# Performance work log

Measured on AMD Instinct MI355X. Metric: run time of the kernel, lower is better.

Reference implementation:

```python
import jax, jax.numpy as jnp
import numpy as np

# Lorentz hyperboloid with curvature -1 (k = 1): <x,x>_L = -1/k, x0 = time coord.
K_CURV = 1.0
EPS = 1e-8
B, N, D, H = 4, 1024, 1024, 16
HD = D // H  # dim_per_head = 64 (space dims per head)


def _time(space):
    # time coord so the point lies on the hyperboloid
    return jnp.sqrt(jnp.sum(space * space, axis=-1, keepdims=True) + 1.0 / K_CURV)


def _lift(space):
    return jnp.concatenate([_time(space), space], axis=-1)


def _linner(u, v):
    # Minkowski inner product <u,v>_L = -u0 v0 + u_s . v_s
    return jnp.sum(u[..., 1:] * v[..., 1:], axis=-1) - u[..., 0] * v[..., 0]


def _lorentz_layernorm(x, gamma, beta):
    s = x[..., 1:]
    mu = jnp.mean(s, axis=-1, keepdims=True)
    var = jnp.mean((s - mu) ** 2, axis=-1, keepdims=True)
    s = (s - mu) / jnp.sqrt(var + 1e-5) * gamma + beta
    return _lift(s)


def _lorentz_linear(x, W, b):
    # linear on the full Lorentz point -> space part of output, time recomputed
    return _lift(x @ W + b)


def _lresnet(x, y, w):
    # Lorentzian residual: (x + w*y) renormalized back onto the hyperboloid
    z = x + w * y
    denom = jnp.sqrt(jnp.clip(-_linner(z, z), EPS))[..., None]
    return z / (jnp.sqrt(K_CURV) * denom)


def _attention(x, Wq, bq, Wk, bk, Wv, bv, Wo, bo):
    def heads(W, b):
        s = (x @ W + b).reshape(B, N, H, HD).transpose(0, 2, 1, 3)  # [B,H,N,HD]
        return _lift(s)  # per-head Lorentz points [B,H,N,HD+1]

    q, k, v = heads(Wq, bq), heads(Wk, bk), heads(Wv, bv)
    sgn = jnp.concatenate([-jnp.ones((1,), x.dtype), jnp.ones((HD,), x.dtype)])
    # pairwise Minkowski inner products; score = -d_L^2 = 2/k + 2<q,k>_L, scaled
    scores = jnp.einsum('bhqd,bhkd->bhqk', q * sgn, k)
    scores = (2.0 / K_CURV + 2.0 * scores) / np.sqrt(HD).astype(np.float32)
    attn = jax.nn.softmax(scores, axis=-1)
    # Lorentz midpoint aggregation of values
    mid = jnp.einsum('bhqk,bhkd->bhqd', attn, v)
    denom = jnp.sqrt(jnp.clip(-_linner(mid, mid), EPS))[..., None]
    mid = mid / (jnp.sqrt(K_CURV) * denom)  # [B,H,N,HD+1]
    cat = mid.transpose(0, 2, 1, 3).reshape(B, N, H * (HD + 1))  # trans_heads_concat
    return _lift(cat @ Wo + bo)


def reference(x, g1, b1, Wq, bq, Wk, bk, Wv, bv, Wo, bo, g2, b2, Wfc, bfc, Wpj, bpj, w1, w2):
    lx = _lorentz_layernorm(x, g1, b1)
    ax = _attention(lx, Wq, bq, Wk, bk, Wv, bv, Wo, bo)
    x = _lresnet(x, ax, w1)
    h = _lorentz_layernorm(x, g2, b2)
    h = _lorentz_linear(h, Wfc, bfc)                      # [B,N,4D]
    h = _lift(jax.nn.gelu(h[..., 1:], approximate=False))  # LorentzActivation(GELU)
    h = _lorentz_linear(h, Wpj, bpj)                      # [B,N,D]
    return _lresnet(x, h, w2)


def setup_inputs() -> dict:
    key = jax.random.key(0)
    ks = jax.random.split(key, 8)
    sc = 0.02
    f32 = jnp.float32
    xs = jax.random.normal(ks[0], (B, N, D - 1), f32)
    return dict(
        x=_lift(xs),
        g1=jnp.ones((D - 1,), f32), b1=jnp.zeros((D - 1,), f32),
        Wq=sc * jax.random.normal(ks[1], (D, H * HD), f32), bq=jnp.zeros((H * HD,), f32),
        Wk=sc * jax.random.normal(ks[2], (D, H * HD), f32), bk=jnp.zeros((H * HD,), f32),
        Wv=sc * jax.random.normal(ks[3], (D, H * HD), f32), bv=jnp.zeros((H * HD,), f32),
        Wo=sc * jax.random.normal(ks[4], (H * (HD + 1), D - 1), f32), bo=jnp.zeros((D - 1,), f32),
        g2=jnp.ones((D - 1,), f32), b2=jnp.zeros((D - 1,), f32),
        Wfc=sc * jax.random.normal(ks[5], (D, 4 * D - 1), f32), bfc=jnp.zeros((4 * D - 1,), f32),
        Wpj=sc * jax.random.normal(ks[6], (4 * D, D - 1), f32), bpj=jnp.zeros((D - 1,), f32),
        w1=jnp.ones((), f32), w2=jnp.ones((), f32),
    )
```

## Files before the change

kernel.cpp:

```cpp
#include <hip/hip_runtime.h>
#include <math.h>

#define BB 4
#define NN 1024
#define DD 1024
#define HH 16
#define ROWS (BB*NN)

typedef __attribute__((ext_vector_type(8))) short bf16x8;
typedef __attribute__((ext_vector_type(4))) float f32x4;
typedef unsigned short u16;

__device__ __forceinline__ u16 f2bf(float f) {
    union { float f; unsigned u; } v; v.f = f;
    unsigned r = v.u + 0x7fff + ((v.u >> 16) & 1);
    return (u16)(r >> 16);
}
__device__ __forceinline__ float bf2f(u16 u) {
    union { unsigned u; float f; } v; v.u = ((unsigned)u) << 16; return v.f;
}

__device__ __forceinline__ void async16(const void* g, void* l) {
    __builtin_amdgcn_global_load_lds(
        (__attribute__((address_space(1))) void*)(uintptr_t)g,
        (__attribute__((address_space(3))) void*)(uintptr_t)l,
        16, 0, 0);
}

__device__ __forceinline__ float block_reduce_sum(float v, float* sm) {
    #pragma unroll
    for (int o = 32; o > 0; o >>= 1) v += __shfl_down(v, o);
    int lane = threadIdx.x & 63, wid = threadIdx.x >> 6;
    if (lane == 0) sm[wid] = v;
    __syncthreads();
    if (wid == 0) {
        v = (lane < (int)(blockDim.x >> 6)) ? sm[lane] : 0.f;
        #pragma unroll
        for (int o = 2; o > 0; o >>= 1) v += __shfl_down(v, o);
        if (lane == 0) sm[0] = v;
    }
    __syncthreads();
    float r = sm[0];
    __syncthreads();
    return r;
}

__global__ __launch_bounds__(256) void k_pre(
        const float* __restrict__ Wq_, const float* __restrict__ Wk_,
        const float* __restrict__ Wv_, const float* __restrict__ Wo_,
        const float* __restrict__ Wfc_, const float* __restrict__ Wpj_,
        u16* __restrict__ WqkvT, u16* __restrict__ WoT,
        u16* __restrict__ WfcT, u16* __restrict__ WpjT,
        const float* __restrict__ x, const float* __restrict__ g1,
        const float* __restrict__ be1, u16* __restrict__ lnout) {
    __shared__ float t[32][33];
    int bid = blockIdx.x;
    if (bid < 12352) {
        const float* W; u16* out; int K, N, Kpad, Npad, gx;
        if (bid < 1024)      { W = Wq_;  out = WqkvT;            K = 1024; N = 1024; Kpad = 1024; Npad = 1024; gx = 32; }
        else if (bid < 2048) { W = Wk_;  out = WqkvT + 1048576;  K = 1024; N = 1024; Kpad = 1024; Npad = 1024; gx = 32; bid -= 1024; }
        else if (bid < 3072) { W = Wv_;  out = WqkvT + 2097152;  K = 1024; N = 1024; Kpad = 1024; Npad = 1024; gx = 32; bid -= 2048; }
        else if (bid < 4160) { W = Wo_;  out = WoT;              K = 1040; N = 1023; Kpad = 1088; Npad = 1024; gx = 34; bid -= 3072; }
        else if (bid < 8256) { W = Wfc_; out = WfcT;             K = 1024; N = 4095; Kpad = 1024; Npad = 4096; gx = 32; bid -= 4160; }
        else                 { W = Wpj_; out = WpjT;             K = 4096; N = 1023; Kpad = 4096; Npad = 1024; gx = 128; bid -= 8256; }
        int k0 = (bid % gx) * 32, n0 = (bid / gx) * 32;
        int tx = threadIdx.x & 31, ty = threadIdx.x >> 5;
        #pragma unroll
        for (int i = 0; i < 32; i += 8) {
            int k = k0 + ty + i, n = n0 + tx;
            t[ty + i][tx] = (k < K && n < N) ? W[(size_t)k * N + n] : 0.f;
        }
        __syncthreads();
        #pragma unroll
        for (int i = 0; i < 32; i += 8) {
            int n = n0 + ty + i, k = k0 + tx;
            if (n < Npad && k < Kpad) out[(size_t)n * Kpad + k] = f2bf(t[tx][ty + i]);
        }
    } else {
        float* sm = &t[0][0];
        int row = bid - 12352;
        const float* xr = x + (size_t)row * DD;
        u16* orow = lnout + (size_t)row * DD;
        float s = 0.f, ss = 0.f;
        for (int j = threadIdx.x; j < DD - 1; j += blockDim.x) {
            float v = xr[1 + j]; s += v; ss += v * v;
        }
        s = block_reduce_sum(s, sm);
        ss = block_reduce_sum(ss, sm);
        float mu = s / (float)(DD - 1);
        float var = ss / (float)(DD - 1) - mu * mu;
        float rstd = rsqrtf(var + 1e-5f);
        float s2 = 0.f;
        for (int j = threadIdx.x; j < DD - 1; j += blockDim.x) {
            float v = (xr[1 + j] - mu) * rstd * g1[j] + be1[j];
            orow[1 + j] = f2bf(v); s2 += v * v;
        }
        s2 = block_reduce_sum(s2, sm);
        if (threadIdx.x == 0) orow[0] = f2bf(sqrtf(s2 + 1.f));
    }
}


__device__ __forceinline__ void cstore(float* p, float v) { *p = v; }
__device__ __forceinline__ void cstore(u16* p, float v) { *p = f2bf(v); }

template <typename OT>
__global__ __launch_bounds__(256) void k_gemm_mfma(
        const u16* __restrict__ A, const u16* __restrict__ BT,
        const float* __restrict__ bias, int nbias,
        OT* __restrict__ C0, OT* __restrict__ C1,
        int ldc, int ldab, int ksplit, int K) {
    __shared__ __align__(16) u16 As[128 * 64];
    __shared__ __align__(16) u16 Bs[128 * 64];
    int z = blockIdx.z;
    int kbeg = z ? ksplit : 0;
    int kend = z ? K : ksplit;
    OT* C = z ? C1 : C0;
    const float* bs = z ? nullptr : bias;

    int tiles_n = gridDim.x;
    int lin = blockIdx.y * tiles_n + blockIdx.x;
    int width = 8 * tiles_n;
    int group = lin / width;
    int rem = lin - group * width;
    int mm = group * 8 + (rem & 7);
    int nn = rem >> 3;
    int n0 = nn * 128, m0 = mm * 128;

    int tid = threadIdx.x;
    int wave = tid >> 6, lane = tid & 63;
    int quad = lane >> 4, m16 = lane & 15;
    int wm = (wave & 1) * 64, wn = (wave >> 1) * 64;

    f32x4 acc[4][4];
    #pragma unroll
    for (int t = 0; t < 4; ++t)
        #pragma unroll
        for (int u = 0; u < 4; ++u) acc[t][u] = (f32x4){0.f, 0.f, 0.f, 0.f};

    int r8 = lane >> 3;
    int cc = (lane & 7) ^ r8;
    int srow = wave * 32 + r8;
    const u16* ag = A  + (size_t)(m0 + srow) * ldab + cc * 8;
    const u16* bg = BT + (size_t)(n0 + srow) * ldab + cc * 8;
    u16* asl = &As[(wave * 32) * 64];
    u16* bsl = &Bs[(wave * 32) * 64];

    for (int k0 = kbeg; k0 < kend; k0 += 64) {
        __syncthreads();
        #pragma unroll
        for (int j = 0; j < 4; ++j) {
            async16(ag + (size_t)(j * 8) * ldab + k0, asl + (j * 8) * 64);
            async16(bg + (size_t)(j * 8) * ldab + k0, bsl + (j * 8) * 64);
        }
        __syncthreads();
        #pragma unroll
        for (int kk = 0; kk < 2; ++kk) {
            bf16x8 af[4], bfr[4];
            #pragma unroll
            for (int t = 0; t < 4; ++t) {
                int slot = (kk * 4 + quad) ^ (m16 & 7);
                af[t] = *(const bf16x8*)&As[(wm + t * 16 + m16) * 64 + slot * 8];
            }
            #pragma unroll
            for (int u = 0; u < 4; ++u) {
                int slot = (kk * 4 + quad) ^ (m16 & 7);
                bfr[u] = *(const bf16x8*)&Bs[(wn + u * 16 + m16) * 64 + slot * 8];
            }
            #pragma unroll
            for (int t = 0; t < 4; ++t)
                #pragma unroll
                for (int u = 0; u < 4; ++u)
                    acc[t][u] = __builtin_amdgcn_mfma_f32_16x16x32_bf16(af[t], bfr[u], acc[t][u], 0, 0, 0);
        }
    }
    #pragma unroll
    for (int u = 0; u < 4; ++u) {
        int col = n0 + wn + u * 16 + m16;
        float bv = (bs != nullptr && col < nbias) ? bs[col] : 0.f;
        #pragma unroll
        for (int t = 0; t < 4; ++t) {
            #pragma unroll
            for (int r = 0; r < 4; ++r) {
                int row = m0 + wm + t * 16 + quad * 4 + r;
                cstore(C + (size_t)row * ldc + col, acc[t][u][r] + bv);
            }
        }
    }
}

__global__ __launch_bounds__(256) void k_build_heads(
        const u16* __restrict__ qkv,
        const float* __restrict__ bq, const float* __restrict__ bk,
        const float* __restrict__ bv,
        u16* __restrict__ Qp, u16* __restrict__ Kp, u16* __restrict__ V2) {
    int wid = threadIdx.x >> 6, lane = threadIdx.x & 63;
    int idx = blockIdx.x * 4 + wid;
    int h = idx & 15, bn = idx >> 4;
    int b = bn >> 10, n = bn & 1023;
    int sec = blockIdx.y;
    const float* bias = (sec == 0) ? bq : (sec == 1) ? bk : bv;
    float v = bf2f(qkv[(size_t)bn * 3072 + sec * 1024 + h * 64 + lane]) + bias[h * 64 + lane];
    float ss = v * v;
    #pragma unroll
    for (int o = 32; o > 0; o >>= 1) ss += __shfl_xor(ss, o);
    float tcomp = sqrtf(ss + 1.f);
    size_t bhn = (size_t)(b * 16 + h) * 1024 + n;
    if (sec == 0) {
        u16* drow = Qp + bhn * 96;
        drow[1 + lane] = f2bf(v);
        if (lane == 0) drow[0] = f2bf(-tcomp);
        if (lane < 31) drow[65 + lane] = 0;
    } else if (sec == 1) {
        u16* drow = Kp + bhn * 104;
        drow[1 + lane] = f2bf(v);
        if (lane == 0) drow[0] = f2bf(tcomp);
        if (lane < 39) drow[65 + lane] = 0;
    } else {
        u16* base = V2 + ((size_t)(b * 16 + h) * 16 + (n >> 6)) * 6144 + (n & 63);
        base[(1 + lane) * 72] = f2bf(v);
        if (lane == 0) base[0] = f2bf(tcomp);
        if (lane >= 49) base[(16 + lane) * 72] = 0;
    }
}

#define AKS 104
#define AVS 72
#define APS 88
#define KTILE_U16 (64 * AKS)
#define VTILE_U16 6144
#define EXPC 0.36067376f
__global__ __launch_bounds__(256) void k_attn_mfma(
        const u16* __restrict__ Qp, const u16* __restrict__ Kp,
        const u16* __restrict__ V2, u16* __restrict__ cat) {
    __shared__ __align__(16) u16 Klds[2][KTILE_U16];
    __shared__ __align__(16) u16 Vlds[2][VTILE_U16];
    __shared__ __align__(16) u16 Plds[4][16 * APS];
    int tid = threadIdx.x;
    int wave = tid >> 6, lane = tid & 63;
    int quad = lane >> 4, m = lane & 15;
    int bh = blockIdx.y, qt = blockIdx.x;

    const u16* kg = Kp + (size_t)bh * 16 * KTILE_U16;
    const u16* vg = V2 + (size_t)bh * 16 * VTILE_U16;

    bf16x8 aq[2][3];
    #pragma unroll
    for (int g = 0; g < 2; ++g) {
        const u16* qptr = Qp + ((size_t)bh * 1024 + qt * 128 + g * 64 + wave * 16 + m) * 96;
        aq[g][0] = *(const bf16x8*)(qptr + quad * 8);
        aq[g][1] = *(const bf16x8*)(qptr + 32 + quad * 8);
        aq[g][2] = *(const bf16x8*)(qptr + 64 + quad * 8);
    }

    f32x4 O[2][5];
    #pragma unroll
    for (int g = 0; g < 2; ++g)
        #pragma unroll
        for (int i = 0; i < 5; ++i) O[g][i] = (f32x4){0.f, 0.f, 0.f, 0.f};

    auto stage = [&](int kt, int s) {
        const u16* kt_p = kg + kt * KTILE_U16 + lane * 8;
        const u16* vt_p = vg + kt * VTILE_U16 + lane * 8;
        for (int i = wave; i < 25; i += 4) {
            if (i < 13) async16(kt_p + i * 512, &Klds[s][i * 512]);
            else        async16(vt_p + (i - 13) * 512, &Vlds[s][(i - 13) * 512]);
        }
    };

    stage(0, 0);
    for (int kt = 0; kt < 16; ++kt) {
        int cur = kt & 1;
        __syncthreads();
        if (kt < 15) stage(kt + 1, cur ^ 1);
        u16* pw = &Plds[wave][0];
        #pragma unroll
        for (int g = 0; g < 2; ++g) {
            #pragma unroll
            for (int nt = 0; nt < 4; ++nt) {
                f32x4 acc = (f32x4){0.f, 0.f, 0.f, 0.f};
                const u16* kr = &Klds[cur][(nt * 16 + m) * AKS + quad * 8];
                acc = __builtin_amdgcn_mfma_f32_16x16x32_bf16(aq[g][0], *(const bf16x8*)(kr),      acc, 0, 0, 0);
                acc = __builtin_amdgcn_mfma_f32_16x16x32_bf16(aq[g][1], *(const bf16x8*)(kr + 32), acc, 0, 0, 0);
                acc = __builtin_amdgcn_mfma_f32_16x16x32_bf16(aq[g][2], *(const bf16x8*)(kr + 64), acc, 0, 0, 0);
                #pragma unroll
                for (int r = 0; r < 4; ++r) {
                    float p = __builtin_amdgcn_exp2f(fmaf(acc[r], EXPC, EXPC));
                    union { float f; unsigned u; } pv; pv.f = p;
                    pw[(quad * 4 + r) * APS + nt * 16 + m] = (u16)((pv.u + 0x8000u) >> 16);
                }
            }
            #pragma unroll
            for (int kc = 0; kc < 2; ++kc) {
                bf16x8 ap = *(const bf16x8*)&Plds[wave][m * APS + kc * 32 + quad * 8];
                #pragma unroll
                for (int vt = 0; vt < 5; ++vt) {
                    bf16x8 bv = *(const bf16x8*)&Vlds[cur][(vt * 16 + m) * AVS + kc * 32 + quad * 8];
                    O[g][vt] = __builtin_amdgcn_mfma_f32_16x16x32_bf16(ap, bv, O[g][vt], 0, 0, 0);
                }
            }
        }
    }
    int b = bh >> 4, h = bh & 15;
    #pragma unroll
    for (int g = 0; g < 2; ++g) {
        #pragma unroll
        for (int r = 0; r < 4; ++r) {
            float part = 0.f;
            #pragma unroll
            for (int vt = 0; vt < 5; ++vt) {
                int c = vt * 16 + m;
                float o = O[g][vt][r];
                part += (c == 0) ? o * o : -o * o;
            }
            part += __shfl_xor(part, 1);
            part += __shfl_xor(part, 2);
            part += __shfl_xor(part, 4);
            part += __shfl_xor(part, 8);
            float rden = rsqrtf(fmaxf(part, 1e-8f));
            int n = qt * 128 + g * 64 + wave * 16 + quad * 4 + r;
            u16* crow = cat + (size_t)(b * 1024 + n) * 1088 + h * 65;
            #pragma unroll
            for (int vt = 0; vt < 5; ++vt) {
                int c = vt * 16 + m;
                if (c < 65) crow[c] = f2bf(O[g][vt][r] * rden);
            }
        }
    }
    if (h == 15) {
        for (int i = tid; i < 128 * 48; i += 256) {
            int rr = i / 48, c = i - rr * 48;
            int n = qt * 128 + rr;
            cat[(size_t)(b * 1024 + n) * 1088 + 1040 + c] = 0;
        }
    }
}

__global__ __launch_bounds__(256) void k_lresnet_ln(
        const float* __restrict__ x, const float* __restrict__ y0,
        const float* __restrict__ y1, const float* __restrict__ wscale,
        const float* __restrict__ g2, const float* __restrict__ be2,
        float* __restrict__ x1, u16* __restrict__ lnout) {
    __shared__ float sm[8];
    int row = blockIdx.x;
    const float* xr = x + (size_t)row * DD;
    const float* ya = y0 + (size_t)row * 1024;
    const float* yb = y1 + (size_t)row * 1024;
    float w = *wscale;
    float zreg[4];
    float sy = 0.f, sz = 0.f, szs = 0.f;
    int cnt = 0;
    for (int j = threadIdx.x; j < DD - 1; j += blockDim.x) {
        float yv = ya[j] + yb[j];
        float zv = xr[1 + j] + w * yv;
        sy += yv * yv; sz += zv * zv; szs += zv;
        zreg[cnt++] = zv;
    }
    sy = block_reduce_sum(sy, sm);
    sz = block_reduce_sum(sz, sm);
    szs = block_reduce_sum(szs, sm);
    float y0t = sqrtf(sy + 1.f);
    float z0 = xr[0] + w * y0t;
    float q = z0 * z0 - sz;
    float rden = rsqrtf(fmaxf(q, 1e-8f));
    float mu = rden * szs / (float)(DD - 1);
    float ex2 = rden * rden * sz / (float)(DD - 1);
    float var = ex2 - mu * mu;
    float rstd = rsqrtf(var + 1e-5f);
    float s2 = 0.f;
    cnt = 0;
    float* x1r = x1 + (size_t)row * DD;
    u16* lr = lnout + (size_t)row * DD;
    for (int j = threadIdx.x; j < DD - 1; j += blockDim.x) {
        float xv = zreg[cnt++] * rden;
        x1r[1 + j] = xv;
        float v = (xv - mu) * rstd * g2[j] + be2[j];
        lr[1 + j] = f2bf(v); s2 += v * v;
    }
    s2 = block_reduce_sum(s2, sm);
    if (threadIdx.x == 0) {
        x1r[0] = z0 * rden;
        lr[0] = f2bf(sqrtf(s2 + 1.f));
    }
}

__global__ __launch_bounds__(256) void k_lresnet(
        const float* __restrict__ x, const float* __restrict__ y0,
        const float* __restrict__ y1, const float* __restrict__ wscale,
        float* __restrict__ out) {
    __shared__ float sm[8];
    int row = blockIdx.x;
    const float* xr = x + (size_t)row * DD;
    const float* ya = y0 + (size_t)row * 1024;
    const float* yb = y1 + (size_t)row * 1024;
    float w = *wscale;
    float zreg[4];
    float sy = 0.f, sz = 0.f;
    int cnt = 0;
    for (int j = threadIdx.x; j < DD - 1; j += blockDim.x) {
        float yv = ya[j] + yb[j];
        float zv = xr[1 + j] + w * yv;
        sy += yv * yv; sz += zv * zv;
        zreg[cnt++] = zv;
    }
    sy = block_reduce_sum(sy, sm);
    sz = block_reduce_sum(sz, sm);
    float y0t = sqrtf(sy + 1.f);
    float z0 = xr[0] + w * y0t;
    float q = z0 * z0 - sz;
    float rden = rsqrtf(fmaxf(q, 1e-8f));
    cnt = 0;
    for (int j = threadIdx.x; j < DD - 1; j += blockDim.x)
        out[(size_t)row * DD + 1 + j] = zreg[cnt++] * rden;
    if (threadIdx.x == 0) out[(size_t)row * DD] = z0 * rden;
}

__global__ __launch_bounds__(256) void k_gelu_lift(
        const u16* __restrict__ hfc, u16* __restrict__ hg) {
    __shared__ float sm[8];
    int row = blockIdx.x;
    const u16* hr = hfc + (size_t)row * 4096;
    u16* gr = hg + (size_t)row * 4096;
    float s2 = 0.f;
    for (int j = threadIdx.x; j < 4095; j += blockDim.x) {
        float v = bf2f(hr[j]);
        float gl = 0.5f * v * (1.f + erff(v * 0.70710678f));
        gr[1 + j] = f2bf(gl); s2 += gl * gl;
    }
    s2 = block_reduce_sum(s2, sm);
    if (threadIdx.x == 0) gr[0] = f2bf(sqrtf(s2 + 1.f));
}

extern "C" void kernel_launch(void* const* d_in, const int* in_sizes, int n_in,
                              void* d_out, int out_size, void* d_ws, size_t ws_size,
                              hipStream_t stream) {
    const float* x   = (const float*)d_in[0];
    const float* g1  = (const float*)d_in[1];
    const float* b1  = (const float*)d_in[2];
    const float* Wq  = (const float*)d_in[3];
    const float* bq  = (const float*)d_in[4];
    const float* Wk  = (const float*)d_in[5];
    const float* bk  = (const float*)d_in[6];
    const float* Wv  = (const float*)d_in[7];
    const float* bv  = (const float*)d_in[8];
    const float* Wo  = (const float*)d_in[9];
    const float* bo  = (const float*)d_in[10];
    const float* g2  = (const float*)d_in[11];
    const float* b2  = (const float*)d_in[12];
    const float* Wfc = (const float*)d_in[13];
    const float* bfc = (const float*)d_in[14];
    const float* Wpj = (const float*)d_in[15];
    const float* bpj = (const float*)d_in[16];
    const float* w1  = (const float*)d_in[17];
    const float* w2  = (const float*)d_in[18];
    float* out = (float*)d_out;

    char* W = (char*)d_ws;
    u16* lx_bf  = (u16*)(W + 0);
    u16* WqkvT  = (u16*)(W + 8388608);
    u16* WoT    = (u16*)(W + 14680064);
    u16* WfcT   = (u16*)(W + 16908288);
    u16* WpjT   = (u16*)(W + 25296896);
    u16* qkv_bf = (u16*)(W + 33685504);
    u16* Qp     = (u16*)(W + 58851328);
    u16* Kp     = (u16*)(W + 71434240);
    u16* V2     = (u16*)(W + 85065728);
    u16* cat_bf = (u16*)(W + 97648640);
    float* ax0  = (float*)(W + 33685504);
    float* ax1  = (float*)(W + 50462720);
    float* x1   = (float*)(W + 67239936);
    u16* hfc_bf = (u16*)(W + 84017152);
    u16* hg_bf  = (u16*)(W + 33685504);
    float* h2a  = (float*)(W + 84017152);
    float* h2b  = (float*)(W + 100794368);

    dim3 blk(256);

    k_pre<<<16448, blk, 0, stream>>>(Wq, Wk, Wv, Wo, Wfc, Wpj,
                                     WqkvT, WoT, WfcT, WpjT,
                                     x, g1, b1, lx_bf);

    k_gemm_mfma<u16><<<dim3(24, 32, 1), blk, 0, stream>>>(
        lx_bf, WqkvT, nullptr, 0, qkv_bf, qkv_bf, 3072, 1024, 1024, 1024);
    k_build_heads<<<dim3(ROWS * HH / 4, 3), blk, 0, stream>>>(
        qkv_bf, bq, bk, bv, Qp, Kp, V2);

    k_attn_mfma<<<dim3(8, 64), blk, 0, stream>>>(Qp, Kp, V2, cat_bf);

    k_gemm_mfma<float><<<dim3(8, 32, 2), blk, 0, stream>>>(
        cat_bf, WoT, bo, 1023, ax0, ax1, 1024, 1088, 576, 1088);

    k_lresnet_ln<<<ROWS, blk, 0, stream>>>(x, ax0, ax1, w1, g2, b2, x1, lx_bf);

    k_gemm_mfma<u16><<<dim3(32, 32, 1), blk, 0, stream>>>(
        lx_bf, WfcT, bfc, 4095, hfc_bf, hfc_bf, 4096, 1024, 1024, 1024);

    k_gelu_lift<<<ROWS, blk, 0, stream>>>(hfc_bf, hg_bf);

    k_gemm_mfma<float><<<dim3(8, 32, 2), blk, 0, stream>>>(
        hg_bf, WpjT, bpj, 1023, h2a, h2b, 1024, 4096, 2048, 4096);

    k_lresnet<<<ROWS, blk, 0, stream>>>(x1, h2a, h2b, w2, out);
}
```

Measured before the change: 446.6 us.

## Double-buffer LDS tiles in MFMA GEMM and drop grouped tile ordering

Splits the GEMM's shared-memory A/B tiles into two stages. The global-to-LDS async load for the next K-tile is issued right after a single barrier, so it overlaps the MFMA work on the current tile; this removes one barrier per iteration and hides load latency. It also replaces the grouped (8-row super-tile) block-to-tile mapping with plain blockIdx mapping, which may reduce L2 reuse across neighbouring blocks. The doubled LDS footprint (64 KB per block) can lower occupancy.

```diff
diff --git a/kernel.cpp b/kernel.cpp
--- a/kernel.cpp
+++ b/kernel.cpp
@@ -100,7 +100,6 @@
     }
 }
 
-
 __device__ __forceinline__ void cstore(float* p, float v) { *p = v; }
 __device__ __forceinline__ void cstore(u16* p, float v) { *p = f2bf(v); }
 
@@ -110,26 +109,18 @@
         const float* __restrict__ bias, int nbias,
         OT* __restrict__ C0, OT* __restrict__ C1,
         int ldc, int ldab, int ksplit, int K) {
-    __shared__ __align__(16) u16 As[128 * 64];
-    __shared__ __align__(16) u16 Bs[128 * 64];
+    __shared__ __align__(16) u16 As[2][128 * 64];
+    __shared__ __align__(16) u16 Bs[2][128 * 64];
     int z = blockIdx.z;
     int kbeg = z ? ksplit : 0;
     int kend = z ? K : ksplit;
     OT* C = z ? C1 : C0;
     const float* bs = z ? nullptr : bias;
 
-    int tiles_n = gridDim.x;
-    int lin = blockIdx.y * tiles_n + blockIdx.x;
-    int width = 8 * tiles_n;
-    int group = lin / width;
-    int rem = lin - group * width;
-    int mm = group * 8 + (rem & 7);
-    int nn = rem >> 3;
-    int n0 = nn * 128, m0 = mm * 128;
-
     int tid = threadIdx.x;
     int wave = tid >> 6, lane = tid & 63;
     int quad = lane >> 4, m16 = lane & 15;
+    int n0 = blockIdx.x * 128, m0 = blockIdx.y * 128;
     int wm = (wave & 1) * 64, wn = (wave >> 1) * 64;
 
     f32x4 acc[4][4];
@@ -143,29 +134,33 @@
     int srow = wave * 32 + r8;
     const u16* ag = A  + (size_t)(m0 + srow) * ldab + cc * 8;
     const u16* bg = BT + (size_t)(n0 + srow) * ldab + cc * 8;
-    u16* asl = &As[(wave * 32) * 64];
-    u16* bsl = &Bs[(wave * 32) * 64];
-
-    for (int k0 = kbeg; k0 < kend; k0 += 64) {
+
+    auto stage = [&](int k0, int s) {
+        #pragma unroll
+        for (int j = 0; j < 4; ++j) {
+            async16(ag + (size_t)(j * 8) * ldab + k0, &As[s][(wave * 32 + j * 8) * 64]);
+            async16(bg + (size_t)(j * 8) * ldab + k0, &Bs[s][(wave * 32 + j * 8) * 64]);
+        }
+    };
+
+    int niter = (kend - kbeg) >> 6;
+    stage(kbeg, 0);
+    for (int it = 0; it < niter; ++it) {
+        int cur = it & 1;
         __syncthreads();
-        #pragma unroll
-        for (int j = 0; j < 4; ++j) {
-            async16(ag + (size_t)(j * 8) * ldab + k0, asl + (j * 8) * 64);
-            async16(bg + (size_t)(j * 8) * ldab + k0, bsl + (j * 8) * 64);
-        }
-        __syncthreads();
+        if (it + 1 < niter) stage(kbeg + (it + 1) * 64, cur ^ 1);
         #pragma unroll
         for (int kk = 0; kk < 2; ++kk) {
             bf16x8 af[4], bfr[4];
             #pragma unroll
             for (int t = 0; t < 4; ++t) {
                 int slot = (kk * 4 + quad) ^ (m16 & 7);
-                af[t] = *(const bf16x8*)&As[(wm + t * 16 + m16) * 64 + slot * 8];
+                af[t] = *(const bf16x8*)&As[cur][(wm + t * 16 + m16) * 64 + slot * 8];
             }
             #pragma unroll
             for (int u = 0; u < 4; ++u) {
                 int slot = (kk * 4 + quad) ^ (m16 & 7);
-                bfr[u] = *(const bf16x8*)&Bs[(wn + u * 16 + m16) * 64 + slot * 8];
+                bfr[u] = *(const bf16x8*)&Bs[cur][(wn + u * 16 + m16) * 64 + slot * 8];
             }
             #pragma unroll
             for (int t = 0; t < 4; ++t)
```

New measurement: 441.9 us. Within noise of the previous version (-1.1%).
